# Optimization experiments

Hardware: AMD Instinct MI355X
Metric: run time of the kernel (lower is better)

## Reference

```python
import jax, jax.numpy as jnp
import numpy as np

G = 256          # grid side -> V = G*G = 65536 nodes
N_BATCH = 4
DIM = 128
N_LAYERS = 2
BN_EPS = 1e-5


def _grid_edges(g):
    # 4-neighbor grid, directed edges both ways; row-normalized weights 1/deg(row)
    idx = np.arange(g * g).reshape(g, g)
    right = np.stack([idx[:, :-1].ravel(), idx[:, 1:].ravel()], axis=0)
    down = np.stack([idx[:-1, :].ravel(), idx[1:, :].ravel()], axis=0)
    und = np.concatenate([right, down], axis=1)
    rows = np.concatenate([und[0], und[1]])
    cols = np.concatenate([und[1], und[0]])
    deg = np.bincount(rows, minlength=g * g).astype(np.float32)
    w = 1.0 / deg[rows]
    return rows.astype(np.int32), cols.astype(np.int32), w.astype(np.float32)


def setup_inputs() -> dict:
    key = jax.random.key(0)
    k_h, k_ws, k_wn = jax.random.split(key, 3)
    rows, cols, w = _grid_edges(G)
    V = G * G
    scale = 1.0 / np.sqrt(DIM)
    return {
        "H": jax.random.normal(k_h, (N_BATCH, V, DIM), dtype=jnp.float32),
        "edge_rows": jnp.asarray(rows),
        "edge_cols": jnp.asarray(cols),
        "edge_w": jnp.asarray(w),
        "Ws": jax.random.normal(k_ws, (N_LAYERS, DIM, DIM), dtype=jnp.float32) * scale,
        "Wn": jax.random.normal(k_wn, (N_LAYERS, DIM, DIM), dtype=jnp.float32) * scale,
        "gamma": jnp.ones((N_LAYERS, DIM), dtype=jnp.float32),
        "beta": jnp.zeros((N_LAYERS, DIM), dtype=jnp.float32),
    }


def reference(H, edge_rows, edge_cols, edge_w, Ws, Wn, gamma, beta):
    N, V, D = H.shape
    X = H
    for l in range(Ws.shape[0]):
        # sparse A_norm @ X[n] for every n, via gather + weighted scatter-add
        msgs = X[:, edge_cols, :] * edge_w[None, :, None]          # [N, E, D]
        X_nei = jnp.zeros_like(X).at[:, edge_rows, :].add(msgs)    # [N, V, D]
        # w_self(X) + w_nei(X_nei); nn.Linear applies x @ W.T
        Y = jnp.einsum("nvd,ed->nve", X, Ws[l]) + jnp.einsum("nvd,ed->nve", X_nei, Wn[l])
        # BatchNorm1d over flattened (N*V) rows, training-mode batch stats
        Yf = Y.reshape(-1, D)
        mean = jnp.mean(Yf, axis=0)
        var = jnp.mean(jnp.square(Yf - mean), axis=0)  # biased variance
        Yn = (Yf - mean) * jax.lax.rsqrt(var + BN_EPS) * gamma[l] + beta[l]
        X = jax.nn.relu(Yn).reshape(N, V, D)
    return X
```

## Files before the change

### kernel.cpp

```cpp
#include <hip/hip_runtime.h>
#include <stdint.h>

#define GS   256
#define VN   65536
#define DD   128
#define MROWSF 262144.0f
#define EPS  1e-5f

typedef __bf16 bf16x8 __attribute__((ext_vector_type(8)));
typedef float  f32x4  __attribute__((ext_vector_type(4)));

__device__ __forceinline__ unsigned short f2bf(float f) {
    union { float f; unsigned int u; } v; v.f = f;
    return (unsigned short)((v.u + 0x7fffu + ((v.u >> 16) & 1u)) >> 16);
}
__device__ __forceinline__ float bf2f(unsigned short u) {
    union { unsigned int u; float f; } v; v.u = ((unsigned int)u) << 16;
    return v.f;
}

__device__ __forceinline__ int sw_u16(int row, int chunk) {
    return row * 256 + (((chunk) ^ (row & 7)) << 3);
}

__global__ __launch_bounds__(256) void prep_w(const float* __restrict__ Ws,
                                              const float* __restrict__ Wn,
                                              unsigned short* __restrict__ Wc) {
    int idx = blockIdx.x * 256 + threadIdx.x;
    int k = idx & 255;
    int n = (idx >> 8) & 127;
    int l = idx >> 15;
    float v = (k < DD) ? Ws[(l * DD + n) * DD + k]
                       : Wn[(l * DD + n) * DD + (k - DD)];
    Wc[idx] = f2bf(v);
}

template<bool APPLY> struct RawV            { using T = float4;  };
template<>           struct RawV<true>      { using T = ushort4; };

template<bool APPLY, bool DSTBF>
__global__ __launch_bounds__(256, 4) void gnn_layer(
    const void* __restrict__ src, const float* __restrict__ affine,
    const unsigned short* __restrict__ Wc, void* __restrict__ dstY,
    float* __restrict__ Pbuf)
{
    using RT = typename RawV<APPLY>::T;
    __shared__ unsigned short A2[64 * 256];
    const int t  = threadIdx.x;
    const int b  = blockIdx.x;
    const int nb = b >> 10;
    const int v0 = (b & 1023) << 6;
    const int r  = v0 >> 8;
    const int c0 = v0 & 255;
    const int q  = t & 31;

    float4 sc = make_float4(0.f, 0.f, 0.f, 0.f), sh = sc;
    if (APPLY) {
        sc = reinterpret_cast<const float4*>(affine)[q];
        sh = reinterpret_cast<const float4*>(affine + DD)[q];
    }
    const size_t base_n = (size_t)nb * VN * DD;
    const RT* __restrict__ srcv = reinterpret_cast<const RT*>(src);

    auto cvt = [&](RT u) -> float4 {
        float4 x;
        if (APPLY) {
            const ushort4& s = *reinterpret_cast<const ushort4*>(&u);
            x.x = fmaxf(bf2f(s.x) * sc.x + sh.x, 0.f);
            x.y = fmaxf(bf2f(s.y) * sc.y + sh.y, 0.f);
            x.z = fmaxf(bf2f(s.z) * sc.z + sh.z, 0.f);
            x.w = fmaxf(bf2f(s.w) * sc.w + sh.w, 0.f);
        } else {
            x = *reinterpret_cast<const float4*>(&u);
        }
        return x;
    };
    auto lds_self = [&](int row) -> float4 {
        ushort4 u = *reinterpret_cast<const ushort4*>(&A2[sw_u16(row, q >> 1) + ((q & 1) << 2)]);
        float4 x; x.x = bf2f(u.x); x.y = bf2f(u.y); x.z = bf2f(u.z); x.w = bf2f(u.w);
        return x;
    };

    const int i0 = t >> 5;
    const bool hasu = (r > 0), hasd = (r < GS - 1);
    const float degr = (hasu ? 1.f : 0.f) + (hasd ? 1.f : 0.f);

    RT sraw[8], uraw[8], draw[8];
    #pragma unroll
    for (int it = 0; it < 8; ++it) {
        const int i = i0 + (it << 3);
        const size_t e4 = (base_n + (size_t)(v0 + i) * DD) >> 2;
        const size_t eq = e4 + q;
        sraw[it] = srcv[eq];
        if (hasu) uraw[it] = srcv[eq - (GS * DD / 4)]; else uraw[it] = RT{};
        if (hasd) draw[it] = srcv[eq + (GS * DD / 4)]; else draw[it] = RT{};
    }

    #pragma unroll
    for (int it = 0; it < 8; ++it) {
        const int i = i0 + (it << 3);
        float4 xs = cvt(sraw[it]);
        ushort4 us;
        us.x = f2bf(xs.x); us.y = f2bf(xs.y); us.z = f2bf(xs.z); us.w = f2bf(xs.w);
        *reinterpret_cast<ushort4*>(&A2[sw_u16(i, q >> 1) + ((q & 1) << 2)]) = us;
    }
    float4 ud[8];
    #pragma unroll
    for (int it = 0; it < 8; ++it) {
        float4 uu = cvt(uraw[it]);
        float4 dd = cvt(draw[it]);
        ud[it] = make_float4(uu.x + dd.x, uu.y + dd.y, uu.z + dd.z, uu.w + dd.w);
    }
    __syncthreads();

    #pragma unroll
    for (int it = 0; it < 8; ++it) {
        const int i = i0 + (it << 3);
        const int c = c0 + i;
        const size_t eq = ((base_n + (size_t)(v0 + i) * DD) >> 2) + q;
        float4 l = make_float4(0.f, 0.f, 0.f, 0.f), rt = l;
        if (i > 0)             l  = lds_self(i - 1);
        else if (c0 > 0)       l  = cvt(srcv[eq - (DD / 4)]);
        if (i < 63)            rt = lds_self(i + 1);
        else if (c0 + 64 < GS) rt = cvt(srcv[eq + (DD / 4)]);
        const float degf = degr + (c > 0 ? 1.f : 0.f) + (c < GS - 1 ? 1.f : 0.f);
        const float wd = 1.f / degf;
        ushort4 un;
        un.x = f2bf((ud[it].x + l.x + rt.x) * wd);
        un.y = f2bf((ud[it].y + l.y + rt.y) * wd);
        un.z = f2bf((ud[it].z + l.z + rt.z) * wd);
        un.w = f2bf((ud[it].w + l.w + rt.w) * wd);
        *reinterpret_cast<ushort4*>(&A2[sw_u16(i, 16 + (q >> 1)) + ((q & 1) << 2)]) = un;
    }
    __syncthreads();

    const int lane = t & 63;
    const int wv   = t >> 6;
    const int lr   = lane & 15;
    const int quad = lane >> 4;

    f32x4 acc[4][2];
    const f32x4 zf = {0.f, 0.f, 0.f, 0.f};
    #pragma unroll
    for (int rt2 = 0; rt2 < 4; ++rt2) { acc[rt2][0] = zf; acc[rt2][1] = zf; }

    const unsigned short* wb0 = Wc + (size_t)((wv << 5) + lr) * 256;
    const unsigned short* wb1 = wb0 + 16 * 256;
    #pragma unroll
    for (int s = 0; s < 8; ++s) {
        const int ck = (s << 2) + quad;
        const bf16x8 b0 = *reinterpret_cast<const bf16x8*>(wb0 + (ck << 3));
        const bf16x8 b1 = *reinterpret_cast<const bf16x8*>(wb1 + (ck << 3));
        #pragma unroll
        for (int rt2 = 0; rt2 < 4; ++rt2) {
            const bf16x8 a = *reinterpret_cast<const bf16x8*>(&A2[sw_u16((rt2 << 4) + lr, ck)]);
            acc[rt2][0] = __builtin_amdgcn_mfma_f32_16x16x32_bf16(a, b0, acc[rt2][0], 0, 0, 0);
            acc[rt2][1] = __builtin_amdgcn_mfma_f32_16x16x32_bf16(a, b1, acc[rt2][1], 0, 0, 0);
        }
    }
    __syncthreads();

    float*          dstf = reinterpret_cast<float*>(dstY) + base_n + (size_t)v0 * DD;
    unsigned short* dstb = reinterpret_cast<unsigned short*>(dstY) + base_n + (size_t)v0 * DD;
    float psum[2] = {0.f, 0.f}, psq[2] = {0.f, 0.f};
    #pragma unroll
    for (int ct = 0; ct < 2; ++ct) {
        const int col = (wv << 5) + (ct << 4) + lr;
        #pragma unroll
        for (int rt2 = 0; rt2 < 4; ++rt2) {
            #pragma unroll
            for (int j = 0; j < 4; ++j) {
                const int row = (rt2 << 4) + (quad << 2) + j;
                const float y = acc[rt2][ct][j];
                if (DSTBF) dstb[row * DD + col] = f2bf(y);
                else       dstf[row * DD + col] = y;
                psum[ct] += y; psq[ct] += y * y;
            }
        }
    }
    float* sred = reinterpret_cast<float*>(A2);
    #pragma unroll
    for (int ct = 0; ct < 2; ++ct) {
        float s1 = psum[ct], s2 = psq[ct];
        s1 += __shfl_xor(s1, 16); s2 += __shfl_xor(s2, 16);
        s1 += __shfl_xor(s1, 32); s2 += __shfl_xor(s2, 32);
        if (quad == 0) {
            const int col = (wv << 5) + (ct << 4) + lr;
            sred[col]      = s1;
            sred[DD + col] = s2;
        }
    }
    __syncthreads();
    Pbuf[(size_t)b * 256 + t] = sred[t];
}

__global__ __launch_bounds__(256) void stats_reduce(const float* __restrict__ P,
                                                    float* __restrict__ P2) {
    const int t = threadIdx.x;
    const float* p = P + (size_t)blockIdx.x * 128 * 256 + t;
    float acc = 0.f;
    #pragma unroll 8
    for (int i = 0; i < 128; ++i) acc += p[(size_t)i * 256];
    P2[(size_t)blockIdx.x * 256 + t] = acc;
}

__global__ void finalize_stats(const float* __restrict__ P2,
                               const float* __restrict__ gamma,
                               const float* __restrict__ beta,
                               float* __restrict__ affine) {
    int f = threadIdx.x;
    if (f < DD) {
        float s1 = 0.f, s2 = 0.f;
        #pragma unroll 8
        for (int j = 0; j < 32; ++j) {
            s1 += P2[j * 256 + f];
            s2 += P2[j * 256 + DD + f];
        }
        const float inv = 1.0f / MROWSF;
        float mean  = s1 * inv;
        float var   = s2 * inv - mean * mean;
        float scale = rsqrtf(var + EPS) * gamma[f];
        affine[f]      = scale;
        affine[DD + f] = beta[f] - mean * scale;
    }
}

template<bool SRCBF>
__global__ __launch_bounds__(256) void final_apply(const void* __restrict__ srcY,
                                                   float* __restrict__ out,
                                                   const float* __restrict__ affine) {
    const int t = threadIdx.x;
    const int q = t & 31;
    const float4 sc = reinterpret_cast<const float4*>(affine)[q];
    const float4 sh = reinterpret_cast<const float4*>(affine + DD)[q];
    size_t idx = (size_t)blockIdx.x * 256 + t;
    #pragma unroll
    for (int it = 0; it < 4; ++it, idx += 2097152) {
        float4 y;
        if (SRCBF) {
            ushort4 u = reinterpret_cast<const ushort4*>(srcY)[idx];
            y.x = bf2f(u.x); y.y = bf2f(u.y); y.z = bf2f(u.z); y.w = bf2f(u.w);
        } else {
            y = reinterpret_cast<const float4*>(srcY)[idx];
        }
        y.x = fmaxf(y.x * sc.x + sh.x, 0.f);
        y.y = fmaxf(y.y * sc.y + sh.y, 0.f);
        y.z = fmaxf(y.z * sc.z + sh.z, 0.f);
        y.w = fmaxf(y.w * sc.w + sh.w, 0.f);
        reinterpret_cast<float4*>(out)[idx] = y;
    }
}

extern "C" void kernel_launch(void* const* d_in, const int* in_sizes, int n_in,
                              void* d_out, int out_size, void* d_ws, size_t ws_size,
                              hipStream_t stream) {
    const float* H     = (const float*)d_in[0];
    const float* Ws    = (const float*)d_in[4];
    const float* Wn    = (const float*)d_in[5];
    const float* gamma = (const float*)d_in[6];
    const float* beta  = (const float*)d_in[7];
    float* out = (float*)d_out;
    char*  ws  = (char*)d_ws;

    unsigned short* Wc = (unsigned short*)ws;
    float* P2   = (float*)(ws + 131072);
    float* aff0 = (float*)(ws + 163840);
    float* aff1 = (float*)(ws + 164864);
    float* Pbuf = (float*)(ws + 165888);
    unsigned short* Y0 = (unsigned short*)(ws + 4360192);
    unsigned short* Y1 = (unsigned short*)(ws + 71469056);
    const bool y1bf = (ws_size >= 138577920);

    prep_w<<<256, 256, 0, stream>>>(Ws, Wn, Wc);
    gnn_layer<false, true ><<<4096, 256, 0, stream>>>((const void*)H, nullptr, Wc, (void*)Y0, Pbuf);
    stats_reduce<<<32, 256, 0, stream>>>(Pbuf, P2);
    finalize_stats<<<1, 128, 0, stream>>>(P2, gamma, beta, aff0);
    if (y1bf) {
        gnn_layer<true, true ><<<4096, 256, 0, stream>>>((const void*)Y0, aff0, Wc + 32768, (void*)Y1, Pbuf);
        stats_reduce<<<32, 256, 0, stream>>>(Pbuf, P2);
        finalize_stats<<<1, 128, 0, stream>>>(P2, gamma + DD, beta + DD, aff1);
        final_apply<true ><<<8192, 256, 0, stream>>>((const void*)Y1, out, aff1);
    } else {
        gnn_layer<true, false><<<4096, 256, 0, stream>>>((const void*)Y0, aff0, Wc + 32768, (void*)out, Pbuf);
        stats_reduce<<<32, 256, 0, stream>>>(Pbuf, P2);
        finalize_stats<<<1, 128, 0, stream>>>(P2, gamma + DD, beta + DD, aff1);
        final_apply<false><<<8192, 256, 0, stream>>>((const void*)out, out, aff1);
    }
}
```

Measured before the change: 380.3 us.

## Use atomic BN stats, prefetch halo and weights, lighter barriers

Replaces the per-block partial-sum buffer plus the separate stats_reduce kernel with global float atomicAdd of per-column sums into a P2 buffer, which prep_w now zeroes. Hoists the left and right halo loads ahead of the LDS stage, software-prefetches the weight fragments across MFMA k-steps, swaps __syncthreads for lgkmcnt-only barriers, and drops one barrier. It also uses the hardware bf16 convert and batches the loads in final_apply. This removes two kernel launches and some latency stalls, at the cost of contention on 256 atomic addresses and non-deterministic summation order.

```diff
diff --git a/kernel.cpp b/kernel.cpp
--- a/kernel.cpp
+++ b/kernel.cpp
@@ -11,22 +11,31 @@
 typedef float  f32x4  __attribute__((ext_vector_type(4)));
 
 __device__ __forceinline__ unsigned short f2bf(float f) {
-    union { float f; unsigned int u; } v; v.f = f;
-    return (unsigned short)((v.u + 0x7fffu + ((v.u >> 16) & 1u)) >> 16);
+    union { __bf16 b; unsigned short u; } v;
+    v.b = (__bf16)f;
+    return v.u;
 }
 __device__ __forceinline__ float bf2f(unsigned short u) {
     union { unsigned int u; float f; } v; v.u = ((unsigned int)u) << 16;
     return v.f;
 }
 
+__device__ __forceinline__ void bar_lds() {
+    asm volatile("s_waitcnt lgkmcnt(0)" ::: "memory");
+    __builtin_amdgcn_s_barrier();
+    asm volatile("" ::: "memory");
+}
+
 __device__ __forceinline__ int sw_u16(int row, int chunk) {
     return row * 256 + (((chunk) ^ (row & 7)) << 3);
 }
 
 __global__ __launch_bounds__(256) void prep_w(const float* __restrict__ Ws,
                                               const float* __restrict__ Wn,
-                                              unsigned short* __restrict__ Wc) {
+                                              unsigned short* __restrict__ Wc,
+                                              float* __restrict__ P2) {
     int idx = blockIdx.x * 256 + threadIdx.x;
+    if (blockIdx.x == 0 && threadIdx.x < 512) P2[threadIdx.x] = 0.f;
     int k = idx & 255;
     int n = (idx >> 8) & 127;
     int l = idx >> 15;
@@ -42,7 +51,7 @@
 __global__ __launch_bounds__(256, 4) void gnn_layer(
     const void* __restrict__ src, const float* __restrict__ affine,
     const unsigned short* __restrict__ Wc, void* __restrict__ dstY,
-    float* __restrict__ Pbuf)
+    float* __restrict__ P2l)
 {
     using RT = typename RawV<APPLY>::T;
     __shared__ unsigned short A2[64 * 256];
@@ -89,12 +98,17 @@
     #pragma unroll
     for (int it = 0; it < 8; ++it) {
         const int i = i0 + (it << 3);
-        const size_t e4 = (base_n + (size_t)(v0 + i) * DD) >> 2;
-        const size_t eq = e4 + q;
+        const size_t eq = ((base_n + (size_t)(v0 + i) * DD) >> 2) + q;
         sraw[it] = srcv[eq];
         if (hasu) uraw[it] = srcv[eq - (GS * DD / 4)]; else uraw[it] = RT{};
         if (hasd) draw[it] = srcv[eq + (GS * DD / 4)]; else draw[it] = RT{};
     }
+    __builtin_amdgcn_sched_barrier(0);
+
+    RT lhraw{}, rhraw{};
+    const size_t eq00 = ((base_n + (size_t)v0 * DD) >> 2) + q;
+    if (i0 == 0 && c0 > 0)       lhraw = srcv[eq00 - (DD / 4)];
+    if (i0 == 7 && c0 + 64 < GS) rhraw = srcv[eq00 + 64 * (DD / 4)];
 
     #pragma unroll
     for (int it = 0; it < 8; ++it) {
@@ -107,22 +121,22 @@
     float4 ud[8];
     #pragma unroll
     for (int it = 0; it < 8; ++it) {
-        float4 uu = cvt(uraw[it]);
-        float4 dd = cvt(draw[it]);
+        float4 uu = make_float4(0.f, 0.f, 0.f, 0.f), dd = uu;
+        if (hasu) uu = cvt(uraw[it]);
+        if (hasd) dd = cvt(draw[it]);
         ud[it] = make_float4(uu.x + dd.x, uu.y + dd.y, uu.z + dd.z, uu.w + dd.w);
     }
-    __syncthreads();
+    bar_lds();
 
     #pragma unroll
     for (int it = 0; it < 8; ++it) {
         const int i = i0 + (it << 3);
         const int c = c0 + i;
-        const size_t eq = ((base_n + (size_t)(v0 + i) * DD) >> 2) + q;
         float4 l = make_float4(0.f, 0.f, 0.f, 0.f), rt = l;
         if (i > 0)             l  = lds_self(i - 1);
-        else if (c0 > 0)       l  = cvt(srcv[eq - (DD / 4)]);
+        else if (c0 > 0)       l  = cvt(lhraw);
         if (i < 63)            rt = lds_self(i + 1);
-        else if (c0 + 64 < GS) rt = cvt(srcv[eq + (DD / 4)]);
+        else if (c0 + 64 < GS) rt = cvt(rhraw);
         const float degf = degr + (c > 0 ? 1.f : 0.f) + (c < GS - 1 ? 1.f : 0.f);
         const float wd = 1.f / degf;
         ushort4 un;
@@ -132,7 +146,6 @@
         un.w = f2bf((ud[it].w + l.w + rt.w) * wd);
         *reinterpret_cast<ushort4*>(&A2[sw_u16(i, 16 + (q >> 1)) + ((q & 1) << 2)]) = un;
     }
-    __syncthreads();
 
     const int lane = t & 63;
     const int wv   = t >> 6;
@@ -146,19 +159,25 @@
 
     const unsigned short* wb0 = Wc + (size_t)((wv << 5) + lr) * 256;
     const unsigned short* wb1 = wb0 + 16 * 256;
+    bf16x8 b0 = *reinterpret_cast<const bf16x8*>(wb0 + (quad << 3));
+    bf16x8 b1 = *reinterpret_cast<const bf16x8*>(wb1 + (quad << 3));
+    bar_lds();
+
     #pragma unroll
     for (int s = 0; s < 8; ++s) {
         const int ck = (s << 2) + quad;
-        const bf16x8 b0 = *reinterpret_cast<const bf16x8*>(wb0 + (ck << 3));
-        const bf16x8 b1 = *reinterpret_cast<const bf16x8*>(wb1 + (ck << 3));
         #pragma unroll
         for (int rt2 = 0; rt2 < 4; ++rt2) {
             const bf16x8 a = *reinterpret_cast<const bf16x8*>(&A2[sw_u16((rt2 << 4) + lr, ck)]);
             acc[rt2][0] = __builtin_amdgcn_mfma_f32_16x16x32_bf16(a, b0, acc[rt2][0], 0, 0, 0);
             acc[rt2][1] = __builtin_amdgcn_mfma_f32_16x16x32_bf16(a, b1, acc[rt2][1], 0, 0, 0);
         }
-    }
-    __syncthreads();
+        if (s < 7) {
+            const int ckn = ((s + 1) << 2) + quad;
+            b0 = *reinterpret_cast<const bf16x8*>(wb0 + (ckn << 3));
+            b1 = *reinterpret_cast<const bf16x8*>(wb1 + (ckn << 3));
+        }
+    }
 
     float*          dstf = reinterpret_cast<float*>(dstY) + base_n + (size_t)v0 * DD;
     unsigned short* dstb = reinterpret_cast<unsigned short*>(dstY) + base_n + (size_t)v0 * DD;
@@ -178,7 +197,6 @@
             }
         }
     }
-    float* sred = reinterpret_cast<float*>(A2);
     #pragma unroll
     for (int ct = 0; ct < 2; ++ct) {
         float s1 = psum[ct], s2 = psq[ct];
@@ -186,39 +204,21 @@
         s1 += __shfl_xor(s1, 32); s2 += __shfl_xor(s2, 32);
         if (quad == 0) {
             const int col = (wv << 5) + (ct << 4) + lr;
-            sred[col]      = s1;
-            sred[DD + col] = s2;
-        }
-    }
-    __syncthreads();
-    Pbuf[(size_t)b * 256 + t] = sred[t];
-}
-
-__global__ __launch_bounds__(256) void stats_reduce(const float* __restrict__ P,
-                                                    float* __restrict__ P2) {
-    const int t = threadIdx.x;
-    const float* p = P + (size_t)blockIdx.x * 128 * 256 + t;
-    float acc = 0.f;
-    #pragma unroll 8
-    for (int i = 0; i < 128; ++i) acc += p[(size_t)i * 256];
-    P2[(size_t)blockIdx.x * 256 + t] = acc;
-}
-
-__global__ void finalize_stats(const float* __restrict__ P2,
+            atomicAdd(P2l + col, s1);
+            atomicAdd(P2l + DD + col, s2);
+        }
+    }
+}
+
+__global__ void finalize_stats(const float* __restrict__ P2l,
                                const float* __restrict__ gamma,
                                const float* __restrict__ beta,
                                float* __restrict__ affine) {
     int f = threadIdx.x;
     if (f < DD) {
-        float s1 = 0.f, s2 = 0.f;
-        #pragma unroll 8
-        for (int j = 0; j < 32; ++j) {
-            s1 += P2[j * 256 + f];
-            s2 += P2[j * 256 + DD + f];
-        }
         const float inv = 1.0f / MROWSF;
-        float mean  = s1 * inv;
-        float var   = s2 * inv - mean * mean;
+        float mean  = P2l[f] * inv;
+        float var   = P2l[DD + f] * inv - mean * mean;
         float scale = rsqrtf(var + EPS) * gamma[f];
         affine[f]      = scale;
         affine[DD + f] = beta[f] - mean * scale;
@@ -233,21 +233,31 @@
     const int q = t & 31;
     const float4 sc = reinterpret_cast<const float4*>(affine)[q];
     const float4 sh = reinterpret_cast<const float4*>(affine + DD)[q];
-    size_t idx = (size_t)blockIdx.x * 256 + t;
-    #pragma unroll
-    for (int it = 0; it < 4; ++it, idx += 2097152) {
-        float4 y;
-        if (SRCBF) {
-            ushort4 u = reinterpret_cast<const ushort4*>(srcY)[idx];
-            y.x = bf2f(u.x); y.y = bf2f(u.y); y.z = bf2f(u.z); y.w = bf2f(u.w);
-        } else {
-            y = reinterpret_cast<const float4*>(srcY)[idx];
-        }
-        y.x = fmaxf(y.x * sc.x + sh.x, 0.f);
-        y.y = fmaxf(y.y * sc.y + sh.y, 0.f);
-        y.z = fmaxf(y.z * sc.z + sh.z, 0.f);
-        y.w = fmaxf(y.w * sc.w + sh.w, 0.f);
-        reinterpret_cast<float4*>(out)[idx] = y;
+    const size_t idx0 = (size_t)blockIdx.x * 256 + t;
+    float4 y[4];
+    if (SRCBF) {
+        ushort4 u[4];
+        #pragma unroll
+        for (int it = 0; it < 4; ++it)
+            u[it] = reinterpret_cast<const ushort4*>(srcY)[idx0 + (size_t)it * 2097152];
+        #pragma unroll
+        for (int it = 0; it < 4; ++it) {
+            y[it].x = bf2f(u[it].x); y[it].y = bf2f(u[it].y);
+            y[it].z = bf2f(u[it].z); y[it].w = bf2f(u[it].w);
+        }
+    } else {
+        #pragma unroll
+        for (int it = 0; it < 4; ++it)
+            y[it] = reinterpret_cast<const float4*>(srcY)[idx0 + (size_t)it * 2097152];
+    }
+    #pragma unroll
+    for (int it = 0; it < 4; ++it) {
+        float4 v = y[it];
+        v.x = fmaxf(v.x * sc.x + sh.x, 0.f);
+        v.y = fmaxf(v.y * sc.y + sh.y, 0.f);
+        v.z = fmaxf(v.z * sc.z + sh.z, 0.f);
+        v.w = fmaxf(v.w * sc.w + sh.w, 0.f);
+        reinterpret_cast<float4*>(out)[idx0 + (size_t)it * 2097152] = v;
     }
 }
 
@@ -266,24 +276,20 @@
     float* P2   = (float*)(ws + 131072);
     float* aff0 = (float*)(ws + 163840);
     float* aff1 = (float*)(ws + 164864);
-    float* Pbuf = (float*)(ws + 165888);
     unsigned short* Y0 = (unsigned short*)(ws + 4360192);
     unsigned short* Y1 = (unsigned short*)(ws + 71469056);
     const bool y1bf = (ws_size >= 138577920);
 
-    prep_w<<<256, 256, 0, stream>>>(Ws, Wn, Wc);
-    gnn_layer<false, true ><<<4096, 256, 0, stream>>>((const void*)H, nullptr, Wc, (void*)Y0, Pbuf);
-    stats_reduce<<<32, 256, 0, stream>>>(Pbuf, P2);
+    prep_w<<<256, 256, 0, stream>>>(Ws, Wn, Wc, P2);
+    gnn_layer<false, true ><<<4096, 256, 0, stream>>>((const void*)H, nullptr, Wc, (void*)Y0, P2);
     finalize_stats<<<1, 128, 0, stream>>>(P2, gamma, beta, aff0);
     if (y1bf) {
-        gnn_layer<true, true ><<<4096, 256, 0, stream>>>((const void*)Y0, aff0, Wc + 32768, (void*)Y1, Pbuf);
-        stats_reduce<<<32, 256, 0, stream>>>(Pbuf, P2);
-        finalize_stats<<<1, 128, 0, stream>>>(P2, gamma + DD, beta + DD, aff1);
+        gnn_layer<true, true ><<<4096, 256, 0, stream>>>((const void*)Y0, aff0, Wc + 32768, (void*)Y1, P2 + 256);
+        finalize_stats<<<1, 128, 0, stream>>>(P2 + 256, gamma + DD, beta + DD, aff1);
         final_apply<true ><<<8192, 256, 0, stream>>>((const void*)Y1, out, aff1);
     } else {
-        gnn_layer<true, false><<<4096, 256, 0, stream>>>((const void*)Y0, aff0, Wc + 32768, (void*)out, Pbuf);
-        stats_reduce<<<32, 256, 0, stream>>>(Pbuf, P2);
-        finalize_stats<<<1, 128, 0, stream>>>(P2, gamma + DD, beta + DD, aff1);
+        gnn_layer<true, false><<<4096, 256, 0, stream>>>((const void*)Y0, aff0, Wc + 32768, (void*)out, P2 + 256);
+        finalize_stats<<<1, 128, 0, stream>>>(P2 + 256, gamma + DD, beta + DD, aff1);
         final_apply<false><<<8192, 256, 0, stream>>>((const void*)out, out, aff1);
     }
 }
```

Result: slower. 459.8 us (+20.9%).

## Swizzle block order, prefetch halo rows early, batch loads in final apply

Applied to the files above, without the earlier changes.

Block IDs are remapped so that blocks landing on the same XCD (round-robin by 8) handle contiguous tiles, which should improve L2 reuse of the up/down neighbor rows. The left/right halo loads are issued up front with the other global loads rather than inside the aggregation loop, so their latency overlaps. final_apply now issues all four loads before any compute, and f2bf uses the native __bf16 conversion. The stats buffer stays indexed by hardware block ID, so the partial sums keep their original layout while the swizzle changes which tile each block processes.

```diff
diff --git a/kernel.cpp b/kernel.cpp
--- a/kernel.cpp
+++ b/kernel.cpp
@@ -11,8 +11,9 @@
 typedef float  f32x4  __attribute__((ext_vector_type(4)));
 
 __device__ __forceinline__ unsigned short f2bf(float f) {
-    union { float f; unsigned int u; } v; v.f = f;
-    return (unsigned short)((v.u + 0x7fffu + ((v.u >> 16) & 1u)) >> 16);
+    union { __bf16 b; unsigned short u; } v;
+    v.b = (__bf16)f;
+    return v.u;
 }
 __device__ __forceinline__ float bf2f(unsigned short u) {
     union { unsigned int u; float f; } v; v.u = ((unsigned int)u) << 16;
@@ -47,7 +48,7 @@
     using RT = typename RawV<APPLY>::T;
     __shared__ unsigned short A2[64 * 256];
     const int t  = threadIdx.x;
-    const int b  = blockIdx.x;
+    const int b  = ((blockIdx.x & 7) << 9) | (blockIdx.x >> 3);
     const int nb = b >> 10;
     const int v0 = (b & 1023) << 6;
     const int r  = v0 >> 8;
@@ -89,12 +90,15 @@
     #pragma unroll
     for (int it = 0; it < 8; ++it) {
         const int i = i0 + (it << 3);
-        const size_t e4 = (base_n + (size_t)(v0 + i) * DD) >> 2;
-        const size_t eq = e4 + q;
+        const size_t eq = ((base_n + (size_t)(v0 + i) * DD) >> 2) + q;
         sraw[it] = srcv[eq];
         if (hasu) uraw[it] = srcv[eq - (GS * DD / 4)]; else uraw[it] = RT{};
         if (hasd) draw[it] = srcv[eq + (GS * DD / 4)]; else draw[it] = RT{};
     }
+    RT lhraw{}, rhraw{};
+    const size_t eq00 = ((base_n + (size_t)v0 * DD) >> 2) + q;
+    if (i0 == 0 && c0 > 0)       lhraw = srcv[eq00 - (DD / 4)];
+    if (i0 == 7 && c0 + 64 < GS) rhraw = srcv[eq00 + 64 * (DD / 4)];
 
     #pragma unroll
     for (int it = 0; it < 8; ++it) {
@@ -117,12 +121,11 @@
     for (int it = 0; it < 8; ++it) {
         const int i = i0 + (it << 3);
         const int c = c0 + i;
-        const size_t eq = ((base_n + (size_t)(v0 + i) * DD) >> 2) + q;
         float4 l = make_float4(0.f, 0.f, 0.f, 0.f), rt = l;
         if (i > 0)             l  = lds_self(i - 1);
-        else if (c0 > 0)       l  = cvt(srcv[eq - (DD / 4)]);
+        else if (c0 > 0)       l  = cvt(lhraw);
         if (i < 63)            rt = lds_self(i + 1);
-        else if (c0 + 64 < GS) rt = cvt(srcv[eq + (DD / 4)]);
+        else if (c0 + 64 < GS) rt = cvt(rhraw);
         const float degf = degr + (c > 0 ? 1.f : 0.f) + (c < GS - 1 ? 1.f : 0.f);
         const float wd = 1.f / degf;
         ushort4 un;
@@ -191,7 +194,7 @@
         }
     }
     __syncthreads();
-    Pbuf[(size_t)b * 256 + t] = sred[t];
+    Pbuf[(size_t)blockIdx.x * 256 + t] = sred[t];
 }
 
 __global__ __launch_bounds__(256) void stats_reduce(const float* __restrict__ P,
@@ -233,21 +236,31 @@
     const int q = t & 31;
     const float4 sc = reinterpret_cast<const float4*>(affine)[q];
     const float4 sh = reinterpret_cast<const float4*>(affine + DD)[q];
-    size_t idx = (size_t)blockIdx.x * 256 + t;
-    #pragma unroll
-    for (int it = 0; it < 4; ++it, idx += 2097152) {
-        float4 y;
-        if (SRCBF) {
-            ushort4 u = reinterpret_cast<const ushort4*>(srcY)[idx];
-            y.x = bf2f(u.x); y.y = bf2f(u.y); y.z = bf2f(u.z); y.w = bf2f(u.w);
-        } else {
-            y = reinterpret_cast<const float4*>(srcY)[idx];
-        }
-        y.x = fmaxf(y.x * sc.x + sh.x, 0.f);
-        y.y = fmaxf(y.y * sc.y + sh.y, 0.f);
-        y.z = fmaxf(y.z * sc.z + sh.z, 0.f);
-        y.w = fmaxf(y.w * sc.w + sh.w, 0.f);
-        reinterpret_cast<float4*>(out)[idx] = y;
+    const size_t idx0 = (size_t)blockIdx.x * 256 + t;
+    float4 y[4];
+    if (SRCBF) {
+        ushort4 u[4];
+        #pragma unroll
+        for (int it = 0; it < 4; ++it)
+            u[it] = reinterpret_cast<const ushort4*>(srcY)[idx0 + (size_t)it * 2097152];
+        #pragma unroll
+        for (int it = 0; it < 4; ++it) {
+            y[it].x = bf2f(u[it].x); y[it].y = bf2f(u[it].y);
+            y[it].z = bf2f(u[it].z); y[it].w = bf2f(u[it].w);
+        }
+    } else {
+        #pragma unroll
+        for (int it = 0; it < 4; ++it)
+            y[it] = reinterpret_cast<const float4*>(srcY)[idx0 + (size_t)it * 2097152];
+    }
+    #pragma unroll
+    for (int it = 0; it < 4; ++it) {
+        float4 v = y[it];
+        v.x = fmaxf(v.x * sc.x + sh.x, 0.f);
+        v.y = fmaxf(v.y * sc.y + sh.y, 0.f);
+        v.z = fmaxf(v.z * sc.z + sh.z, 0.f);
+        v.w = fmaxf(v.w * sc.w + sh.w, 0.f);
+        reinterpret_cast<float4*>(out)[idx0 + (size_t)it * 2097152] = v;
     }
 }
 
```

After: 390.1 us. 2.6% more time.
